# Performance work log

Hardware: AMD Instinct MI355X
Metric: run time of the kernel (lower is better)

## Reference

```python
import jax, jax.numpy as jnp
import numpy as np

B, T, D, H = 256, 512, 128, 64


def _gru_dir(x_tbd, Wi, Wh, bi, bh):
    # PyTorch GRU semantics. x_tbd: [T,B,D]; Wi: [3H,D]; Wh: [3H,H].
    xg = jnp.einsum('tbd,gd->tbg', x_tbd, Wi) + bi  # [T,B,3H]

    def step(h, xg_t):
        hg = h @ Wh.T + bh
        xr, xz, xn = jnp.split(xg_t, 3, axis=-1)
        hr, hz, hn = jnp.split(hg, 3, axis=-1)
        r = jax.nn.sigmoid(xr + hr)
        z = jax.nn.sigmoid(xz + hz)
        n = jnp.tanh(xn + r * hn)
        h = (1.0 - z) * n + z * h
        return h, h

    h0 = jnp.zeros((x_tbd.shape[1], Wh.shape[1]), x_tbd.dtype)
    _, hs = jax.lax.scan(step, h0, xg)
    return hs  # [T,B,H]


def _hb_dir(x_tbd, W, b, U, c):
    # Custom HBLSTM cell. W: [D,5H] (input proj), U: [H,5H] (hidden proj).
    # Gate order: f, i, o, u, k. Both biases folded into the x projection.
    xp = jnp.einsum('tbd,dg->tbg', x_tbd, W) + b + c  # [T,B,5H]

    def step(carry, xp_t):
        h, k, kp = carry
        pre = xp_t + h @ U
        f, i, o, u, kc = jnp.split(pre, 5, axis=-1)
        f = jax.nn.sigmoid(f)
        i = jax.nn.sigmoid(i)
        o = jax.nn.sigmoid(o)
        u = jax.nn.sigmoid(u)
        kp = u * jnp.tanh(kc) + (1.0 - u) * kp
        k = f * k + i * kp
        h = o * jnp.tanh(k)
        return (h, k, kp), h

    z = jnp.zeros((x_tbd.shape[1], U.shape[0]), x_tbd.dtype)
    _, hs = jax.lax.scan(step, (z, z, z), xp)
    return hs  # [T,B,H]


def _forward(x, gru_f_Wi, gru_f_Wh, gru_f_bi, gru_f_bh,
             gru_b_Wi, gru_b_Wh, gru_b_bi, gru_b_bh,
             hb_f_W, hb_f_b, hb_f_U, hb_f_c,
             hb_b_W, hb_b_b, hb_b_U, hb_b_c,
             fast_W, fast_b, stab_W, stab_b,
             attnp_W, attnp_b, attns_W, attns_b,
             gate_W1, gate_b1, gate_W2, gate_b2,
             head_W1, head_b1, head_W2, head_b2):
    xt = jnp.transpose(x, (1, 0, 2))  # [T,B,D]
    xr = xt[::-1]

    # Fast branch: bidirectional GRU; only last-timestep output is used.
    hf = _gru_dir(xt, gru_f_Wi, gru_f_Wh, gru_f_bi, gru_f_bh)
    hb_ = _gru_dir(xr, gru_b_Wi, gru_b_Wh, gru_b_bi, gru_b_bh)
    # fast_seq[:, -1, :] = [fwd hidden at t=T-1, bwd hidden at t=T-1]
    fast_last = jnp.concatenate([hf[-1], hb_[0]], axis=-1) @ fast_W + fast_b

    # Stable branch: bidirectional HBLSTM.
    sf = _hb_dir(xt, hb_f_W, hb_f_b, hb_f_U, hb_f_c)
    sb = _hb_dir(xr, hb_b_W, hb_b_b, hb_b_U, hb_b_c)[::-1]
    stable_seq = jnp.transpose(jnp.concatenate([sf, sb], axis=-1), (1, 0, 2))  # [B,T,2H]

    # Attention pooling over time.
    attn_hidden = jnp.tanh(stable_seq @ attnp_W + attnp_b)        # [B,T,H]
    logits = (attn_hidden @ attns_W + attns_b)[..., 0]            # [B,T]
    w = jax.nn.softmax(logits, axis=1)
    stable_ctx = jnp.einsum('bt,btd->bd', w, stable_seq)
    stable_ctx = stable_ctx @ stab_W + stab_b                     # [B,2H]

    # Gated fusion (dropout is identity in eval).
    g_in = jnp.concatenate([fast_last, stable_ctx], axis=-1)      # [B,4H]
    g_h = jax.nn.relu(g_in @ gate_W1 + gate_b1)
    gate = jax.nn.sigmoid(g_h @ gate_W2 + gate_b2)                # [B,1]
    fused = gate * fast_last + (1.0 - gate) * stable_ctx

    out = jnp.concatenate([fused, fast_last, stable_ctx], axis=-1)  # [B,6H]
    h1 = jax.nn.relu(out @ head_W1 + head_b1)
    return h1 @ head_W2 + head_b2                                  # [B,1]


def setup_inputs() -> dict:
    key = jax.random.key(0)
    ks = iter(jax.random.split(key, 64))

    def p(shape, fan_in):
        return jax.random.normal(next(ks), shape, dtype=jnp.float32) / np.sqrt(fan_in)

    d = {'x': jax.random.normal(next(ks), (B, T, D), dtype=jnp.float32)}
    for pre in ('gru_f', 'gru_b'):
        d[pre + '_Wi'] = p((3 * H, D), D)
        d[pre + '_Wh'] = p((3 * H, H), H)
        d[pre + '_bi'] = p((3 * H,), H)
        d[pre + '_bh'] = p((3 * H,), H)
    for pre in ('hb_f', 'hb_b'):
        d[pre + '_W'] = p((D, 5 * H), D)
        d[pre + '_b'] = p((5 * H,), D)
        d[pre + '_U'] = p((H, 5 * H), H)
        d[pre + '_c'] = p((5 * H,), H)
    d['fast_W'] = p((2 * H, 2 * H), 2 * H); d['fast_b'] = p((2 * H,), 2 * H)
    d['stab_W'] = p((2 * H, 2 * H), 2 * H); d['stab_b'] = p((2 * H,), 2 * H)
    d['attnp_W'] = p((2 * H, H), 2 * H);   d['attnp_b'] = p((H,), 2 * H)
    d['attns_W'] = p((H, 1), H);           d['attns_b'] = p((1,), H)
    d['gate_W1'] = p((4 * H, 2 * H), 4 * H); d['gate_b1'] = p((2 * H,), 4 * H)
    d['gate_W2'] = p((2 * H, 1), 2 * H);     d['gate_b2'] = p((1,), 2 * H)
    d['head_W1'] = p((6 * H, 2 * H), 6 * H); d['head_b1'] = p((2 * H,), 6 * H)
    d['head_W2'] = p((2 * H, 1), 2 * H);     d['head_b2'] = p((1,), 2 * H)
    return d


def reference(x, gru_f_Wi, gru_f_Wh, gru_f_bi, gru_f_bh,
              gru_b_Wi, gru_b_Wh, gru_b_bi, gru_b_bh,
              hb_f_W, hb_f_b, hb_f_U, hb_f_c,
              hb_b_W, hb_b_b, hb_b_U, hb_b_c,
              fast_W, fast_b, stab_W, stab_b,
              attnp_W, attnp_b, attns_W, attns_b,
              gate_W1, gate_b1, gate_W2, gate_b2,
              head_W1, head_b1, head_W2, head_b2):
    return _forward(x, gru_f_Wi, gru_f_Wh, gru_f_bi, gru_f_bh,
                    gru_b_Wi, gru_b_Wh, gru_b_bi, gru_b_bh,
                    hb_f_W, hb_f_b, hb_f_U, hb_f_c,
                    hb_b_W, hb_b_b, hb_b_U, hb_b_c,
                    fast_W, fast_b, stab_W, stab_b,
                    attnp_W, attnp_b, attns_W, attns_b,
                    gate_W1, gate_b1, gate_W2, gate_b2,
                    head_W1, head_b1, head_W2, head_b2)
```

## Files before the change

### kernel.cpp

```cpp
#include <hip/hip_runtime.h>
#include <math.h>

#define B_ 256
#define T_ 512
#define D_ 128
#define H_ 64

static const size_t F_SF    = 0;
static const size_t F_SB    = F_SF + (size_t)T_ * B_ * 64;
static const size_t F_ST    = F_SB + (size_t)T_ * B_ * 64;
static const size_t F_FASTL = F_ST + (size_t)7 * B_ * 64;
static const size_t F_LOG   = F_FASTL + (size_t)B_ * 128;
static const size_t F_CTX   = F_LOG + (size_t)B_ * T_;
static const size_t F_CHUNK = F_CTX + (size_t)B_ * 128;

__device__ __forceinline__ float sigmoidf_(float x) {
    return 1.0f / (1.0f + __expf(-x));
}
__device__ __forceinline__ float tanhf_(float x) {
    float ax = fabsf(x);
    float e  = __expf(-2.0f * ax);
    float t  = (1.0f - e) / (1.0f + e);
    return copysignf(t, x);
}
__device__ __forceinline__ float rl_(float v, int lane) {
    return __int_as_float(__builtin_amdgcn_readlane(__float_as_int(v), lane));
}
__device__ __forceinline__ float wave_sum(float v) {
#pragma unroll
    for (int off = 32; off > 0; off >>= 1) v += __shfl_xor(v, off);
    return v;
}
__device__ __forceinline__ float wave_max(float v) {
#pragma unroll
    for (int off = 32; off > 0; off >>= 1) v = fmaxf(v, __shfl_xor(v, off));
    return v;
}

#define R32(M) M(0) M(1) M(2) M(3) M(4) M(5) M(6) M(7) \
               M(8) M(9) M(10) M(11) M(12) M(13) M(14) M(15) \
               M(16) M(17) M(18) M(19) M(20) M(21) M(22) M(23) \
               M(24) M(25) M(26) M(27) M(28) M(29) M(30) M(31)

template<int N, bool WGD, bool REV>
__global__ __launch_bounds__(256, 1) void gemm_in(
    const float* __restrict__ x, const float* __restrict__ W,
    const float* __restrict__ b1, const float* __restrict__ b2,
    float* __restrict__ out, int t0)
{
    __shared__ float a_lds[64 * 132];
    __shared__ float w_lds[64 * 68];

    const int tid = threadIdx.x;
    const int tl  = blockIdx.z;
    const int tg  = t0 + tl;
    const int txi = REV ? (T_ - 1 - tg) : tg;
    const int b0  = blockIdx.y * 128;
    const int g0  = blockIdx.x * 64;

    const int ty = tid >> 4, tx = tid & 15;
    float acc[8][4] = {};

    for (int kh = 0; kh < 2; kh++) {
#pragma unroll
        for (int i = 0; i < 8; i++) {
            int flat = i * 256 + tid;
            int r    = flat >> 4;
            int c4   = flat & 15;
            const float4 v = *reinterpret_cast<const float4*>(
                x + ((size_t)(b0 + r) * T_ + txi) * D_ + kh * 64 + c4 * 4);
            const int rs = r ^ ((c4 & 7) << 2);
            a_lds[(c4 * 4 + 0) * 132 + rs] = v.x;
            a_lds[(c4 * 4 + 1) * 132 + rs] = v.y;
            a_lds[(c4 * 4 + 2) * 132 + rs] = v.z;
            a_lds[(c4 * 4 + 3) * 132 + rs] = v.w;
        }
        if (WGD) {
#pragma unroll
            for (int i = 0; i < 4; i++) {
                int flat = i * 256 + tid;
                int r    = flat >> 4;
                int c4   = flat & 15;
                const float4 v = *reinterpret_cast<const float4*>(
                    W + (size_t)(g0 + r) * D_ + kh * 64 + c4 * 4);
                const int rs = r ^ ((c4 & 7) << 2);
                w_lds[(c4 * 4 + 0) * 68 + rs] = v.x;
                w_lds[(c4 * 4 + 1) * 68 + rs] = v.y;
                w_lds[(c4 * 4 + 2) * 68 + rs] = v.z;
                w_lds[(c4 * 4 + 3) * 68 + rs] = v.w;
            }
        } else {
#pragma unroll
            for (int i = 0; i < 4; i++) {
                int flat = i * 256 + tid;
                int k    = flat >> 4;
                int c4   = flat & 15;
                const float4 v = *reinterpret_cast<const float4*>(
                    W + (size_t)(kh * 64 + k) * N + g0 + c4 * 4);
                const int ns = (c4 * 4) ^ (((k >> 2) & 7) << 2);
                *reinterpret_cast<float4*>(&w_lds[k * 68 + ns]) = v;
            }
        }
        __syncthreads();
#pragma unroll 8
        for (int k = 0; k < 64; k++) {
            const int sw = ((k >> 2) & 7) << 2;
            const float4 am0 = *reinterpret_cast<const float4*>(
                &a_lds[k * 132 + ((ty * 8) ^ sw)]);
            const float4 am1 = *reinterpret_cast<const float4*>(
                &a_lds[k * 132 + ((ty * 8 + 4) ^ sw)]);
            const float4 wn4 = *reinterpret_cast<const float4*>(
                &w_lds[k * 68 + ((tx * 4) ^ sw)]);
            const float am[8] = {am0.x, am0.y, am0.z, am0.w,
                                 am1.x, am1.y, am1.z, am1.w};
            const float wn[4] = {wn4.x, wn4.y, wn4.z, wn4.w};
#pragma unroll
            for (int mi = 0; mi < 8; mi++)
#pragma unroll
                for (int ni = 0; ni < 4; ni++)
                    acc[mi][ni] = fmaf(am[mi], wn[ni], acc[mi][ni]);
        }
        __syncthreads();
    }

    float bias[4];
#pragma unroll
    for (int ni = 0; ni < 4; ni++) {
        float bb = b1[g0 + tx * 4 + ni];
        if (b2 != nullptr) bb += b2[g0 + tx * 4 + ni];
        bias[ni] = bb;
    }
#pragma unroll
    for (int mi = 0; mi < 8; mi++) {
        float4 o;
        o.x = acc[mi][0] + bias[0];
        o.y = acc[mi][1] + bias[1];
        o.z = acc[mi][2] + bias[2];
        o.w = acc[mi][3] + bias[3];
        *reinterpret_cast<float4*>(
            out + ((size_t)tl * B_ + b0 + ty * 8 + mi) * N + g0 + tx * 4) = o;
    }
}

__global__ __launch_bounds__(384, 1) void recur(
    const float* __restrict__ xg_c, const float* __restrict__ xpf_c,
    const float* __restrict__ xpb_c,
    const float* __restrict__ gWh, const float* __restrict__ gbh,
    const float* __restrict__ Uf,  const float* __restrict__ Ub,
    float* __restrict__ sf, float* __restrict__ sb,
    float* __restrict__ state, int t0, int C)
{
    __shared__ float hpart[2][2][2][5][64];
    __shared__ float gpart[2][2][3][64];
    const int tid = threadIdx.x;
    const int w   = tid & 63;
    const int wv  = tid >> 6;

    if (wv < 4) {
        const int lc    = wv >> 1;
        const int p     = wv & 1;
        const int jbase = p << 5;
        const int hb    = blockIdx.x * 2 + lc;
        const int dir   = hb >= 256 ? 1 : 0;
        const int batch = hb - (dir ? 256 : 0);
        const float* U  = dir ? Ub : Uf;
        const float* xp = dir ? xpb_c : xpf_c;
        float* outbuf   = dir ? sb : sf;
        float* stH  = state + (size_t)(1 + dir * 3) * B_ * 64;
        float* stK  = stH + (size_t)B_ * 64;
        float* stKp = stK + (size_t)B_ * 64;

        float h, k, kp;
        if (t0 == 0) { h = 0.0f; k = 0.0f; kp = 0.0f; }
        else {
            h  = stH [(size_t)batch * 64 + w];
            k  = stK [(size_t)batch * 64 + w];
            kp = stKp[(size_t)batch * 64 + w];
        }

#define DECL_U(i) float u0_##i, u1_##i, u2_##i, u3_##i, u4_##i;
        R32(DECL_U)
#undef DECL_U
#define LOAD_U(i) { const float* Uj = U + (size_t)(jbase + i) * 320 + w;      \
        u0_##i = Uj[0];   u1_##i = Uj[64];  u2_##i = Uj[128];                 \
        u3_##i = Uj[192]; u4_##i = Uj[256];                                   \
        asm volatile("" : "+v"(u0_##i), "+v"(u1_##i), "+v"(u2_##i),           \
                          "+v"(u3_##i), "+v"(u4_##i)); }
        R32(LOAD_U)
#undef LOAD_U

        float xv0, xv1, xv2, xv3, xv4;
        {
            const float* pp = xp + (size_t)batch * 320;
            xv0 = pp[w]; xv1 = pp[64 + w]; xv2 = pp[128 + w];
            xv3 = pp[192 + w]; xv4 = pp[256 + w];
        }
        for (int t = 0; t < C; t++) {
            float xn0, xn1, xn2, xn3, xn4;
            {
                int tn = (t + 1 < C) ? (t + 1) : t;
                const float* pn = xp + ((size_t)tn * B_ + batch) * 320;
                xn0 = pn[w]; xn1 = pn[64 + w]; xn2 = pn[128 + w];
                xn3 = pn[192 + w]; xn4 = pn[256 + w];
            }
            float a0 = 0.f, a1 = 0.f, a2 = 0.f, a3 = 0.f, a4 = 0.f;
#define ACC_U(i) { const float hj = rl_(h, jbase + i);                        \
        a0 = fmaf(hj, u0_##i, a0); a1 = fmaf(hj, u1_##i, a1);                 \
        a2 = fmaf(hj, u2_##i, a2); a3 = fmaf(hj, u3_##i, a3);                 \
        a4 = fmaf(hj, u4_##i, a4); }
            R32(ACC_U)
#undef ACC_U

            const int bf = t & 1;
            hpart[bf][lc][p][0][w] = a0;
            hpart[bf][lc][p][1][w] = a1;
            hpart[bf][lc][p][2][w] = a2;
            hpart[bf][lc][p][3][w] = a3;
            hpart[bf][lc][p][4][w] = a4;
            __syncthreads();
            a0 += hpart[bf][lc][1 - p][0][w];
            a1 += hpart[bf][lc][1 - p][1][w];
            a2 += hpart[bf][lc][1 - p][2][w];
            a3 += hpart[bf][lc][1 - p][3][w];
            a4 += hpart[bf][lc][1 - p][4][w];

            float f   = sigmoidf_(xv0 + a0);
            float ii  = sigmoidf_(xv1 + a1);
            float o   = sigmoidf_(xv2 + a2);
            float uu  = sigmoidf_(xv3 + a3);
            float tkc = tanhf_(xv4 + a4);
            kp = uu * tkc + (1.0f - uu) * kp;
            k  = f * k + ii * kp;
            h  = o * tanhf_(k);
            if (p == 0) {
                int tg   = t0 + t;
                int tout = dir ? (T_ - 1 - tg) : tg;
                outbuf[((size_t)tout * B_ + batch) * 64 + w] = h;
            }
            xv0 = xn0; xv1 = xn1; xv2 = xn2; xv3 = xn3; xv4 = xn4;
        }
        if (p == 0) {
            stH [(size_t)batch * 64 + w] = h;
            stK [(size_t)batch * 64 + w] = k;
            stKp[(size_t)batch * 64 + w] = kp;
        }
    } else {
        const int p     = wv - 4;
        const int jbase = p << 5;
        const int batch = blockIdx.x;
        float* stH = state;
        float h = (t0 == 0) ? 0.0f : stH[(size_t)batch * 64 + w];

#define DECL_W(i) float wh0_##i, wh1_##i, wh2_##i;
        R32(DECL_W)
#undef DECL_W
#define LOAD_W(i) {                                                           \
        wh0_##i = gWh[(size_t)(0 * 64 + w) * 64 + jbase + i];                 \
        wh1_##i = gWh[(size_t)(1 * 64 + w) * 64 + jbase + i];                 \
        wh2_##i = gWh[(size_t)(2 * 64 + w) * 64 + jbase + i];                 \
        asm volatile("" : "+v"(wh0_##i), "+v"(wh1_##i), "+v"(wh2_##i)); }
        R32(LOAD_W)
#undef LOAD_W
        const float bh0 = gbh[w], bh1 = gbh[64 + w], bh2 = gbh[128 + w];

        float xv0, xv1, xv2;
        {
            const float* pp = xg_c + (size_t)batch * 192;
            xv0 = pp[w]; xv1 = pp[64 + w]; xv2 = pp[128 + w];
        }
        for (int t = 0; t < C; t++) {
            float xn0, xn1, xn2;
            {
                int tn = (t + 1 < C) ? (t + 1) : t;
                const float* pn = xg_c + ((size_t)tn * B_ + batch) * 192;
                xn0 = pn[w]; xn1 = pn[64 + w]; xn2 = pn[128 + w];
            }
            float a0 = 0.f, a1 = 0.f, a2 = 0.f;
#define ACC_W(i) { const float hj = rl_(h, jbase + i);                        \
        a0 = fmaf(hj, wh0_##i, a0); a1 = fmaf(hj, wh1_##i, a1);               \
        a2 = fmaf(hj, wh2_##i, a2); }
            R32(ACC_W)
#undef ACC_W

            const int bf = t & 1;
            gpart[bf][p][0][w] = a0;
            gpart[bf][p][1][w] = a1;
            gpart[bf][p][2][w] = a2;
            __syncthreads();
            a0 += gpart[bf][1 - p][0][w];
            a1 += gpart[bf][1 - p][1][w];
            a2 += gpart[bf][1 - p][2][w];

            float r = sigmoidf_(xv0 + bh0 + a0);
            float z = sigmoidf_(xv1 + bh1 + a1);
            float n = tanhf_(xv2 + r * (bh2 + a2));
            h = (1.0f - z) * n + z * h;
            xv0 = xn0; xv1 = xn1; xv2 = xn2;
        }
        if (p == 0) stH[(size_t)batch * 64 + w] = h;
    }
}

__global__ __launch_bounds__(64) void tail1(
    const float* __restrict__ x, const float* __restrict__ Wib,
    const float* __restrict__ bib, const float* __restrict__ bhb,
    const float* __restrict__ hfl, const float* __restrict__ fW,
    const float* __restrict__ fb, float* __restrict__ fastl)
{
    __shared__ float xrow[128];
    __shared__ float inb[128];
    const int b = blockIdx.x;
    const int l = threadIdx.x;
    xrow[l]      = x[((size_t)b * T_ + (T_ - 1)) * D_ + l];
    xrow[64 + l] = x[((size_t)b * T_ + (T_ - 1)) * D_ + 64 + l];
    inb[l] = hfl[(size_t)b * 64 + l];
    __syncthreads();
    float a0 = bib[l], a1 = bib[64 + l], a2 = bib[128 + l];
#pragma unroll 8
    for (int d = 0; d < 128; d++) {
        float xd = xrow[d];
        a0 = fmaf(xd, Wib[(size_t)l * 128 + d], a0);
        a1 = fmaf(xd, Wib[(size_t)(64 + l) * 128 + d], a1);
        a2 = fmaf(xd, Wib[(size_t)(128 + l) * 128 + d], a2);
    }
    float r = sigmoidf_(a0 + bhb[l]);
    float z = sigmoidf_(a1 + bhb[64 + l]);
    float n = tanhf_(a2 + r * bhb[128 + l]);
    inb[64 + l] = (1.0f - z) * n;
    __syncthreads();
    float acc0 = fb[l], acc1 = fb[64 + l];
#pragma unroll 8
    for (int i2 = 0; i2 < 128; i2++) {
        float v = inb[i2];
        acc0 = fmaf(v, fW[(size_t)i2 * 128 + l], acc0);
        acc1 = fmaf(v, fW[(size_t)i2 * 128 + 64 + l], acc1);
    }
    fastl[(size_t)b * 128 + l]      = acc0;
    fastl[(size_t)b * 128 + 64 + l] = acc1;
}

__global__ __launch_bounds__(256) void attn_logits(
    const float* __restrict__ sf, const float* __restrict__ sb,
    const float* __restrict__ Wp, const float* __restrict__ bp,
    const float* __restrict__ Ws, const float* __restrict__ bs,
    float* __restrict__ logits)
{
    __shared__ float wp_t[64 * 129];
    __shared__ float s_lds[4][132];
    __shared__ float bp_l[64], ws_l[64];
    const int tid = threadIdx.x;
#pragma unroll
    for (int i = 0; i < 32; i++) {
        int idx = i * 256 + tid;
        int d = idx >> 6, g = idx & 63;
        wp_t[g * 129 + d] = Wp[idx];
    }
    if (tid < 64) { bp_l[tid] = bp[tid]; ws_l[tid] = Ws[tid]; }
    __syncthreads();
    const int wave = tid >> 6, l = tid & 63;
    for (int it = 0; it < 64; it++) {
        int p  = blockIdx.x * 256 + wave * 64 + it;
        int bb = p >> 9;
        int t  = p & 511;
        s_lds[wave][l]      = sf[((size_t)t * B_ + bb) * 64 + l];
        s_lds[wave][64 + l] = sb[((size_t)t * B_ + bb) * 64 + l];
        float acc = bp_l[l];
#pragma unroll 8
        for (int d = 0; d < 128; d++)
            acc = fmaf(s_lds[wave][d], wp_t[l * 129 + d], acc);
        float v = tanhf_(acc) * ws_l[l];
        v = wave_sum(v);
        if (l == 0) logits[(size_t)bb * T_ + t] = v + bs[0];
    }
}

__global__ __launch_bounds__(256) void softmax_k(float* __restrict__ logits)
{
    __shared__ float red[8];
    const int b = blockIdx.x, tid = threadIdx.x;
    const int wave = tid >> 6, l = tid & 63;
    float* row = logits + (size_t)b * T_;
    float l0 = row[tid], l1 = row[tid + 256];
    float m = wave_max(fmaxf(l0, l1));
    if (l == 0) red[wave] = m;
    __syncthreads();
    m = fmaxf(fmaxf(red[0], red[1]), fmaxf(red[2], red[3]));
    float e0 = __expf(l0 - m), e1 = __expf(l1 - m);
    float s = wave_sum(e0 + e1);
    if (l == 0) red[4 + wave] = s;
    __syncthreads();
    s = red[4] + red[5] + red[6] + red[7];
    row[tid]       = e0 / s;
    row[tid + 256] = e1 / s;
}

__global__ __launch_bounds__(128) void ctx_k(
    const float* __restrict__ wsm, const float* __restrict__ sf,
    const float* __restrict__ sb, const float* __restrict__ stW,
    const float* __restrict__ stb, float* __restrict__ ctxo)
{
    __shared__ float wrow[512];
    __shared__ float cpre[128];
    const int b = blockIdx.x, tid = threadIdx.x;
#pragma unroll
    for (int i = 0; i < 4; i++) wrow[i * 128 + tid] = wsm[(size_t)b * T_ + i * 128 + tid];
    __syncthreads();
    const float* src = (tid < 64) ? sf : sb;
    const int d = tid & 63;
    float acc = 0.0f;
#pragma unroll 4
    for (int t = 0; t < 512; t++)
        acc = fmaf(wrow[t], src[((size_t)t * B_ + b) * 64 + d], acc);
    cpre[tid] = acc;
    __syncthreads();
    float a2 = stb[tid];
#pragma unroll 8
    for (int i2 = 0; i2 < 128; i2++)
        a2 = fmaf(cpre[i2], stW[(size_t)i2 * 128 + tid], a2);
    ctxo[(size_t)b * 128 + tid] = a2;
}

__global__ __launch_bounds__(128) void tail2(
    const float* __restrict__ fastl, const float* __restrict__ ctxo,
    const float* __restrict__ gW1, const float* __restrict__ gb1,
    const float* __restrict__ gW2, const float* __restrict__ gb2,
    const float* __restrict__ hW1, const float* __restrict__ hb1,
    const float* __restrict__ hW2, const float* __restrict__ hb2,
    float* __restrict__ outp)
{
    __shared__ float gin[256];
    __shared__ float outv[384];
    __shared__ float red2[2];
    const int b = blockIdx.x, tid = threadIdx.x;
    gin[tid]       = fastl[(size_t)b * 128 + tid];
    gin[128 + tid] = ctxo[(size_t)b * 128 + tid];
    __syncthreads();
    float a = gb1[tid];
#pragma unroll 8
    for (int i = 0; i < 256; i++)
        a = fmaf(gin[i], gW1[(size_t)i * 128 + tid], a);
    float gh = fmaxf(a, 0.0f);
    float v = wave_sum(gh * gW2[tid]);
    if ((tid & 63) == 0) red2[tid >> 6] = v;
    __syncthreads();
    float gate = sigmoidf_(red2[0] + red2[1] + gb2[0]);
    float fl = gin[tid], sc = gin[128 + tid];
    outv[tid]       = gate * fl + (1.0f - gate) * sc;
    outv[128 + tid] = fl;
    outv[256 + tid] = sc;
    __syncthreads();
    float a1 = hb1[tid];
#pragma unroll 8
    for (int i = 0; i < 384; i++)
        a1 = fmaf(outv[i], hW1[(size_t)i * 128 + tid], a1);
    float h1v = fmaxf(a1, 0.0f);
    float vv = wave_sum(h1v * hW2[tid]);
    if ((tid & 63) == 0) red2[tid >> 6] = vv;
    __syncthreads();
    if (tid == 0) outp[b] = red2[0] + red2[1] + hb2[0];
}

extern "C" void kernel_launch(void* const* d_in, const int* in_sizes, int n_in,
                              void* d_out, int out_size, void* d_ws, size_t ws_size,
                              hipStream_t stream)
{
    (void)in_sizes; (void)n_in; (void)out_size;
    const float* x      = (const float*)d_in[0];
    const float* gfWi   = (const float*)d_in[1];
    const float* gfWh   = (const float*)d_in[2];
    const float* gfbi   = (const float*)d_in[3];
    const float* gfbh   = (const float*)d_in[4];
    const float* gbWi   = (const float*)d_in[5];
    const float* gbbi   = (const float*)d_in[7];
    const float* gbbh   = (const float*)d_in[8];
    const float* hbfW   = (const float*)d_in[9];
    const float* hbfb   = (const float*)d_in[10];
    const float* hbfU   = (const float*)d_in[11];
    const float* hbfc   = (const float*)d_in[12];
    const float* hbbW   = (const float*)d_in[13];
    const float* hbbb   = (const float*)d_in[14];
    const float* hbbU   = (const float*)d_in[15];
    const float* hbbc   = (const float*)d_in[16];
    const float* fastW  = (const float*)d_in[17];
    const float* fastb  = (const float*)d_in[18];
    const float* stabW  = (const float*)d_in[19];
    const float* stabb  = (const float*)d_in[20];
    const float* attnpW = (const float*)d_in[21];
    const float* attnpb = (const float*)d_in[22];
    const float* attnsW = (const float*)d_in[23];
    const float* attnsb = (const float*)d_in[24];
    const float* gW1    = (const float*)d_in[25];
    const float* gb1    = (const float*)d_in[26];
    const float* gW2    = (const float*)d_in[27];
    const float* gb2    = (const float*)d_in[28];
    const float* hW1    = (const float*)d_in[29];
    const float* hb1    = (const float*)d_in[30];
    const float* hW2    = (const float*)d_in[31];
    const float* hb2    = (const float*)d_in[32];

    float* ws    = (float*)d_ws;
    float* sf    = ws + F_SF;
    float* sb    = ws + F_SB;
    float* st    = ws + F_ST;
    float* fastl = ws + F_FASTL;
    float* logit = ws + F_LOG;
    float* ctxo  = ws + F_CTX;

    const size_t wsf = ws_size / sizeof(float);
    int C = T_;
    while (C > 1 && F_CHUNK + (size_t)C * B_ * 832 > wsf) C >>= 1;
    const int nc = T_ / C;

    float* xg_c  = ws + F_CHUNK;
    float* xpf_c = xg_c  + (size_t)C * B_ * 192;
    float* xpb_c = xpf_c + (size_t)C * B_ * 320;

    for (int c = 0; c < nc; c++) {
        const int t0 = c * C;
        gemm_in<192, true,  false><<<dim3(3, 2, C), 256, 0, stream>>>(x, gfWi, gfbi, nullptr, xg_c, t0);
        gemm_in<320, false, false><<<dim3(5, 2, C), 256, 0, stream>>>(x, hbfW, hbfb, hbfc, xpf_c, t0);
        gemm_in<320, false, true ><<<dim3(5, 2, C), 256, 0, stream>>>(x, hbbW, hbbb, hbbc, xpb_c, t0);
        recur<<<dim3(256), 384, 0, stream>>>(xg_c, xpf_c, xpb_c, gfWh, gfbh, hbfU, hbbU,
                                             sf, sb, st, t0, C);
    }

    tail1<<<dim3(B_), 64, 0, stream>>>(x, gbWi, gbbi, gbbh, st, fastW, fastb, fastl);

    attn_logits<<<dim3(512), 256, 0, stream>>>(sf, sb, attnpW, attnpb, attnsW, attnsb, logit);
    softmax_k<<<dim3(B_), 256, 0, stream>>>(logit);
    ctx_k<<<dim3(B_), 128, 0, stream>>>(logit, sf, sb, stabW, stabb, ctxo);

    tail2<<<dim3(B_), 128, 0, stream>>>(fastl, ctxo, gW1, gb1, gW2, gb2,
                                        hW1, hb1, hW2, hb2, (float*)d_out);
}
```

Measured before the change: 1.577 ms.

## Split recurrence work per gate across waves, one sequence per block

New measurement: 1.658 ms. 1.05x slower.

```diff
diff --git a/kernel.cpp b/kernel.cpp
--- a/kernel.cpp
+++ b/kernel.cpp
@@ -37,10 +37,24 @@
     return v;
 }
 
-#define R32(M) M(0) M(1) M(2) M(3) M(4) M(5) M(6) M(7) \
+#define R64(M) M(0) M(1) M(2) M(3) M(4) M(5) M(6) M(7) \
                M(8) M(9) M(10) M(11) M(12) M(13) M(14) M(15) \
                M(16) M(17) M(18) M(19) M(20) M(21) M(22) M(23) \
-               M(24) M(25) M(26) M(27) M(28) M(29) M(30) M(31)
+               M(24) M(25) M(26) M(27) M(28) M(29) M(30) M(31) \
+               M(32) M(33) M(34) M(35) M(36) M(37) M(38) M(39) \
+               M(40) M(41) M(42) M(43) M(44) M(45) M(46) M(47) \
+               M(48) M(49) M(50) M(51) M(52) M(53) M(54) M(55) \
+               M(56) M(57) M(58) M(59) M(60) M(61) M(62) M(63)
+
+#define ACC64(M) \
+  M(0,p0) M(1,p0) M(2,p0) M(3,p0) M(4,p0) M(5,p0) M(6,p0) M(7,p0) \
+  M(8,p0) M(9,p0) M(10,p0) M(11,p0) M(12,p0) M(13,p0) M(14,p0) M(15,p0) \
+  M(16,p1) M(17,p1) M(18,p1) M(19,p1) M(20,p1) M(21,p1) M(22,p1) M(23,p1) \
+  M(24,p1) M(25,p1) M(26,p1) M(27,p1) M(28,p1) M(29,p1) M(30,p1) M(31,p1) \
+  M(32,p2) M(33,p2) M(34,p2) M(35,p2) M(36,p2) M(37,p2) M(38,p2) M(39,p2) \
+  M(40,p2) M(41,p2) M(42,p2) M(43,p2) M(44,p2) M(45,p2) M(46,p2) M(47,p2) \
+  M(48,p3) M(49,p3) M(50,p3) M(51,p3) M(52,p3) M(53,p3) M(54,p3) M(55,p3) \
+  M(56,p3) M(57,p3) M(58,p3) M(59,p3) M(60,p3) M(61,p3) M(62,p3) M(63,p3)
 
 template<int N, bool WGD, bool REV>
 __global__ __launch_bounds__(256, 1) void gemm_in(
@@ -142,7 +156,7 @@
     }
 }
 
-__global__ __launch_bounds__(384, 1) void recur(
+__global__ __launch_bounds__(512, 4) void recur(
     const float* __restrict__ xg_c, const float* __restrict__ xpf_c,
     const float* __restrict__ xpb_c,
     const float* __restrict__ gWh, const float* __restrict__ gbh,
@@ -150,19 +164,18 @@
     float* __restrict__ sf, float* __restrict__ sb,
     float* __restrict__ state, int t0, int C)
 {
-    __shared__ float hpart[2][2][2][5][64];
-    __shared__ float gpart[2][2][3][64];
+    __shared__ float hv[2][5][64];
+    __shared__ float gv[2][4][64];
     const int tid = threadIdx.x;
     const int w   = tid & 63;
     const int wv  = tid >> 6;
-
-    if (wv < 4) {
-        const int lc    = wv >> 1;
-        const int p     = wv & 1;
-        const int jbase = p << 5;
-        const int hb    = blockIdx.x * 2 + lc;
-        const int dir   = hb >= 256 ? 1 : 0;
-        const int batch = hb - (dir ? 256 : 0);
+    const int typeA = (blockIdx.x < 256);
+
+    if (wv < 5) {
+        const int g     = wv;
+        const int gofs  = g * 64;
+        const int dir   = typeA ? 0 : 1;
+        const int batch = typeA ? blockIdx.x : (blockIdx.x - 256);
         const float* U  = dir ? Ub : Uf;
         const float* xp = dir ? xpb_c : xpf_c;
         float* outbuf   = dir ? sb : sf;
@@ -178,126 +191,98 @@
             kp = stKp[(size_t)batch * 64 + w];
         }
 
-#define DECL_U(i) float u0_##i, u1_##i, u2_##i, u3_##i, u4_##i;
-        R32(DECL_U)
+#define DECL_U(i) float uw_##i;
+        R64(DECL_U)
 #undef DECL_U
-#define LOAD_U(i) { const float* Uj = U + (size_t)(jbase + i) * 320 + w;      \
-        u0_##i = Uj[0];   u1_##i = Uj[64];  u2_##i = Uj[128];                 \
-        u3_##i = Uj[192]; u4_##i = Uj[256];                                   \
-        asm volatile("" : "+v"(u0_##i), "+v"(u1_##i), "+v"(u2_##i),           \
-                          "+v"(u3_##i), "+v"(u4_##i)); }
-        R32(LOAD_U)
+#define LOAD_U(i) uw_##i = U[(size_t)(i) * 320 + gofs + w];                   \
+        asm volatile("" : "+v"(uw_##i));
+        R64(LOAD_U)
 #undef LOAD_U
 
-        float xv0, xv1, xv2, xv3, xv4;
-        {
-            const float* pp = xp + (size_t)batch * 320;
-            xv0 = pp[w]; xv1 = pp[64 + w]; xv2 = pp[128 + w];
-            xv3 = pp[192 + w]; xv4 = pp[256 + w];
-        }
+        float xv = xp[(size_t)batch * 320 + gofs + w];
         for (int t = 0; t < C; t++) {
-            float xn0, xn1, xn2, xn3, xn4;
-            {
-                int tn = (t + 1 < C) ? (t + 1) : t;
-                const float* pn = xp + ((size_t)tn * B_ + batch) * 320;
-                xn0 = pn[w]; xn1 = pn[64 + w]; xn2 = pn[128 + w];
-                xn3 = pn[192 + w]; xn4 = pn[256 + w];
-            }
-            float a0 = 0.f, a1 = 0.f, a2 = 0.f, a3 = 0.f, a4 = 0.f;
-#define ACC_U(i) { const float hj = rl_(h, jbase + i);                        \
-        a0 = fmaf(hj, u0_##i, a0); a1 = fmaf(hj, u1_##i, a1);                 \
-        a2 = fmaf(hj, u2_##i, a2); a3 = fmaf(hj, u3_##i, a3);                 \
-        a4 = fmaf(hj, u4_##i, a4); }
-            R32(ACC_U)
+            int tn = (t + 1 < C) ? (t + 1) : t;
+            float xn = xp[((size_t)tn * B_ + batch) * 320 + gofs + w];
+
+            float p0 = 0.f, p1 = 0.f, p2 = 0.f, p3 = 0.f;
+#define ACC_U(i, acc) { const float hj = rl_(h, i);                           \
+            acc = fmaf(hj, uw_##i, acc); }
+            ACC64(ACC_U)
 #undef ACC_U
-
             const int bf = t & 1;
-            hpart[bf][lc][p][0][w] = a0;
-            hpart[bf][lc][p][1][w] = a1;
-            hpart[bf][lc][p][2][w] = a2;
-            hpart[bf][lc][p][3][w] = a3;
-            hpart[bf][lc][p][4][w] = a4;
+            hv[bf][g][w] = xv + ((p0 + p1) + (p2 + p3));
             __syncthreads();
-            a0 += hpart[bf][lc][1 - p][0][w];
-            a1 += hpart[bf][lc][1 - p][1][w];
-            a2 += hpart[bf][lc][1 - p][2][w];
-            a3 += hpart[bf][lc][1 - p][3][w];
-            a4 += hpart[bf][lc][1 - p][4][w];
-
-            float f   = sigmoidf_(xv0 + a0);
-            float ii  = sigmoidf_(xv1 + a1);
-            float o   = sigmoidf_(xv2 + a2);
-            float uu  = sigmoidf_(xv3 + a3);
-            float tkc = tanhf_(xv4 + a4);
+            const float v0 = hv[bf][0][w];
+            const float v1 = hv[bf][1][w];
+            const float v2 = hv[bf][2][w];
+            const float v3 = hv[bf][3][w];
+            const float v4 = hv[bf][4][w];
+
+            float f   = sigmoidf_(v0);
+            float ii  = sigmoidf_(v1);
+            float o   = sigmoidf_(v2);
+            float uu  = sigmoidf_(v3);
+            float tkc = tanhf_(v4);
             kp = uu * tkc + (1.0f - uu) * kp;
             k  = f * k + ii * kp;
             h  = o * tanhf_(k);
-            if (p == 0) {
-                int tg   = t0 + t;
-                int tout = dir ? (T_ - 1 - tg) : tg;
+            if (g == 0) {
+                int tg2  = t0 + t;
+                int tout = dir ? (T_ - 1 - tg2) : tg2;
                 outbuf[((size_t)tout * B_ + batch) * 64 + w] = h;
             }
-            xv0 = xn0; xv1 = xn1; xv2 = xn2; xv3 = xn3; xv4 = xn4;
-        }
-        if (p == 0) {
+            xv = xn;
+        }
+        if (g == 0) {
             stH [(size_t)batch * 64 + w] = h;
             stK [(size_t)batch * 64 + w] = k;
             stKp[(size_t)batch * 64 + w] = kp;
         }
-    } else {
-        const int p     = wv - 4;
-        const int jbase = p << 5;
+    } else if (typeA) {
+        const int g     = wv - 5;
+        const int gofs  = g * 64;
         const int batch = blockIdx.x;
         float* stH = state;
+
         float h = (t0 == 0) ? 0.0f : stH[(size_t)batch * 64 + w];
-
-#define DECL_W(i) float wh0_##i, wh1_##i, wh2_##i;
-        R32(DECL_W)
+        const float bh = gbh[gofs + w];
+
+#define DECL_W(i) float wh_##i;
+        R64(DECL_W)
 #undef DECL_W
-#define LOAD_W(i) {                                                           \
-        wh0_##i = gWh[(size_t)(0 * 64 + w) * 64 + jbase + i];                 \
-        wh1_##i = gWh[(size_t)(1 * 64 + w) * 64 + jbase + i];                 \
-        wh2_##i = gWh[(size_t)(2 * 64 + w) * 64 + jbase + i];                 \
-        asm volatile("" : "+v"(wh0_##i), "+v"(wh1_##i), "+v"(wh2_##i)); }
-        R32(LOAD_W)
+#define LOAD_W(i) wh_##i = gWh[(size_t)(gofs + w) * 64 + (i)];                \
+        asm volatile("" : "+v"(wh_##i));
+        R64(LOAD_W)
 #undef LOAD_W
-        const float bh0 = gbh[w], bh1 = gbh[64 + w], bh2 = gbh[128 + w];
-
-        float xv0, xv1, xv2;
-        {
-            const float* pp = xg_c + (size_t)batch * 192;
-            xv0 = pp[w]; xv1 = pp[64 + w]; xv2 = pp[128 + w];
-        }
+
+        float xv = xg_c[(size_t)batch * 192 + gofs + w];
         for (int t = 0; t < C; t++) {
-            float xn0, xn1, xn2;
-            {
-                int tn = (t + 1 < C) ? (t + 1) : t;
-                const float* pn = xg_c + ((size_t)tn * B_ + batch) * 192;
-                xn0 = pn[w]; xn1 = pn[64 + w]; xn2 = pn[128 + w];
+            int tn = (t + 1 < C) ? (t + 1) : t;
+            float xn = xg_c[((size_t)tn * B_ + batch) * 192 + gofs + w];
+
+            float p0 = 0.f, p1 = 0.f, p2 = 0.f, p3 = 0.f;
+#define ACC_W(i, acc) { const float hj = rl_(h, i);                           \
+            acc = fmaf(hj, wh_##i, acc); }
+            ACC64(ACC_W)
+#undef ACC_W
+            const float a = (p0 + p1) + (p2 + p3);
+            const int bf = t & 1;
+            if (g < 2) {
+                gv[bf][g][w] = xv + bh + a;
+            } else {
+                gv[bf][2][w] = bh + a;
+                gv[bf][3][w] = xv;
             }
-            float a0 = 0.f, a1 = 0.f, a2 = 0.f;
-#define ACC_W(i) { const float hj = rl_(h, jbase + i);                        \
-        a0 = fmaf(hj, wh0_##i, a0); a1 = fmaf(hj, wh1_##i, a1);               \
-        a2 = fmaf(hj, wh2_##i, a2); }
-            R32(ACC_W)
-#undef ACC_W
-
-            const int bf = t & 1;
-            gpart[bf][p][0][w] = a0;
-            gpart[bf][p][1][w] = a1;
-            gpart[bf][p][2][w] = a2;
             __syncthreads();
-            a0 += gpart[bf][1 - p][0][w];
-            a1 += gpart[bf][1 - p][1][w];
-            a2 += gpart[bf][1 - p][2][w];
-
-            float r = sigmoidf_(xv0 + bh0 + a0);
-            float z = sigmoidf_(xv1 + bh1 + a1);
-            float n = tanhf_(xv2 + r * (bh2 + a2));
+            float r = sigmoidf_(gv[bf][0][w]);
+            float z = sigmoidf_(gv[bf][1][w]);
+            float n = tanhf_(gv[bf][3][w] + r * gv[bf][2][w]);
             h = (1.0f - z) * n + z * h;
-            xv0 = xn0; xv1 = xn1; xv2 = xn2;
-        }
-        if (p == 0) stH[(size_t)batch * 64 + w] = h;
+            xv = xn;
+        }
+        if (g == 0) stH[(size_t)batch * 64 + w] = h;
+    } else {
+        for (int t = 0; t < C; t++) __syncthreads();
     }
 }
 
@@ -520,7 +505,7 @@
         gemm_in<192, true,  false><<<dim3(3, 2, C), 256, 0, stream>>>(x, gfWi, gfbi, nullptr, xg_c, t0);
         gemm_in<320, false, false><<<dim3(5, 2, C), 256, 0, stream>>>(x, hbfW, hbfb, hbfc, xpf_c, t0);
         gemm_in<320, false, true ><<<dim3(5, 2, C), 256, 0, stream>>>(x, hbbW, hbbb, hbbc, xpb_c, t0);
-        recur<<<dim3(256), 384, 0, stream>>>(xg_c, xpf_c, xpb_c, gfWh, gfbh, hbfU, hbbU,
+        recur<<<dim3(512), 512, 0, stream>>>(xg_c, xpf_c, xpb_c, gfWh, gfbh, hbfU, hbbU,
                                              sf, sb, st, t0, C);
     }
 
```
